# Optimization experiments

Hardware: AMD Instinct MI355X
Metric: run time of the kernel (lower is better)

The kernel has to match this reference:

```python
import math
import jax, jax.numpy as jnp
import numpy as np

B, LQ, LK, D, H = 4, 2048, 2048, 512, 8  # dim_Q=dim_K=dim_V=D, num_heads=H


def _layernorm(x, g, b, eps=1e-5):
    mu = jnp.mean(x, axis=-1, keepdims=True)
    var = jnp.var(x, axis=-1, keepdims=True)
    return (x - mu) * jax.lax.rsqrt(var + eps) * g + b


def setup_inputs() -> dict:
    key = jax.random.key(0)
    ks = jax.random.split(key, 16)
    s = 1.0 / math.sqrt(D)
    return {
        "Q": jax.random.normal(ks[0], (B, LQ, D), jnp.float32),
        "K": jax.random.normal(ks[1], (B, LK, D), jnp.float32),
        "pad_mask": jax.random.randint(ks[2], (B, LK), 0, 2, jnp.int32),
        "Wq": jax.random.normal(ks[3], (D, D), jnp.float32) * s,
        "bq": jnp.zeros((D,), jnp.float32),
        "Wk": jax.random.normal(ks[4], (D, D), jnp.float32) * s,
        "bk": jnp.zeros((D,), jnp.float32),
        "Wv": jax.random.normal(ks[5], (D, D), jnp.float32) * s,
        "bv": jnp.zeros((D,), jnp.float32),
        "Wo": jax.random.normal(ks[6], (D, D), jnp.float32) * s,
        "bo": jnp.zeros((D,), jnp.float32),
        "g0": jnp.ones((D,), jnp.float32),
        "b0": jnp.zeros((D,), jnp.float32),
        "g1": jnp.ones((D,), jnp.float32),
        "b1": jnp.zeros((D,), jnp.float32),
    }


def reference(Q, K, pad_mask, Wq, bq, Wk, bk, Wv, bv, Wo, bo, g0, b0, g1, b1):
    d = D // H  # head dim (torch: split(dim_split, 2) then cat along batch)
    Qh = (Q @ Wq + bq).reshape(B, LQ, H, d)
    Kh = (K @ Wk + bk).reshape(B, LK, H, d)
    Vh = (K @ Wv + bv).reshape(B, LK, H, d)
    # NOTE: original scales by sqrt(dim_V), not sqrt(head_dim)
    score = jnp.einsum('bqhd,bkhd->bhqk', Qh, Kh) / np.float32(math.sqrt(D))
    m = pad_mask[:, None, None, :].astype(score.dtype)  # (B,1,1,Lk)
    score = jnp.where(m == 0, jnp.float32(-1e12), score)
    A = jax.nn.softmax(score, axis=-1) * m  # post-softmax mask multiply (faithful)
    O = jnp.einsum('bhqk,bkhd->bqhd', A, Vh).reshape(B, LQ, D)
    O = Q + O
    O = _layernorm(O, g0, b0)
    O = O + jax.nn.relu(O @ Wo + bo)
    O = _layernorm(O, g1, b1)
    return O
```

## Files before the change

kernel.cpp:

```cpp
#include <hip/hip_runtime.h>
#include <math.h>

#define NB   4
#define SLQ  2048
#define SLK  2048
#define DIM  512
#define NH   8
#define HD   64
#define NROWS (NB * SLQ)
#define NT   (SLK / 64)

typedef __attribute__((ext_vector_type(8)))  __bf16 bf16x8;
typedef __attribute__((ext_vector_type(4)))  __bf16 bf16x4;
typedef __attribute__((ext_vector_type(2)))  __bf16 bf16x2;
typedef __attribute__((ext_vector_type(4)))  float  f32x4;
typedef __attribute__((ext_vector_type(16))) float  f32x16;
typedef __attribute__((ext_vector_type(4)))  unsigned int u32x4;

typedef const __attribute__((address_space(1))) void* as1_cptr;
typedef __attribute__((address_space(3))) void*       as3_ptr;
__device__ __forceinline__ void async_ld16(const void* g, void* s) {
    __builtin_amdgcn_global_load_lds((as1_cptr)g, (as3_ptr)s, 16, 0, 0);
}

__global__ __launch_bounds__(256)
void transpose_w_kernel(const float* __restrict__ Wq, const float* __restrict__ Wk,
                        const float* __restrict__ Wv, const float* __restrict__ Wo,
                        const int* __restrict__ maskp,
                        __bf16* __restrict__ Wt, float* __restrict__ msentg) {
    const int m = blockIdx.z;
    const int t = threadIdx.x;
    if (m == 4) {
        const int idx = (blockIdx.y * 16 + blockIdx.x) * 256 + t;
        if (idx < NB * SLK) msentg[idx] = maskp[idx] ? 0.f : -1e30f;
        return;
    }
    __shared__ float Ls[32][33];
    const float* W = (m == 0) ? Wq : (m == 1) ? Wk : (m == 2) ? Wv : Wo;
    const int k0 = blockIdx.y * 32, n0 = blockIdx.x * 32;
    const int r  = t >> 3, c = (t & 7) * 4;

    const float4 v = *reinterpret_cast<const float4*>(&W[(size_t)(k0 + r) * DIM + n0 + c]);
    Ls[r][c + 0] = v.x; Ls[r][c + 1] = v.y; Ls[r][c + 2] = v.z; Ls[r][c + 3] = v.w;
    __syncthreads();

    const int n = t >> 3, k = (t & 7) * 4;
    bf16x4 o;
    o[0] = (__bf16)Ls[k + 0][n];
    o[1] = (__bf16)Ls[k + 1][n];
    o[2] = (__bf16)Ls[k + 2][n];
    o[3] = (__bf16)Ls[k + 3][n];
    *reinterpret_cast<bf16x4*>(&Wt[(size_t)(512 * m + n0 + n) * DIM + k0 + k]) = o;
}

__global__ __launch_bounds__(256)
void proj_mfma_kernel(const float* __restrict__ Qp, const float* __restrict__ Kp,
                      const __bf16* __restrict__ Wt,
                      const float* __restrict__ bq, const float* __restrict__ bk,
                      const float* __restrict__ bv,
                      __bf16* __restrict__ Qh, __bf16* __restrict__ Kh,
                      __bf16* __restrict__ VhT) {
    __shared__ __bf16 As[128][72];
    __shared__ __bf16 Bs[64][72];

    const int bx = blockIdx.x;
    const int mode = (bx < 8) ? 0 : (bx < 16) ? 1 : 2;
    const int cb   = bx - ((mode == 0) ? 0 : (mode == 1) ? 8 : 16);
    const float*  A    = (mode == 0) ? Qp : Kp;
    const __bf16* Bt   = Wt + (size_t)((mode == 0) ? 0 : (mode == 1) ? 512 : 1024) * DIM;
    const float*  bias = ((mode == 0) ? bq : (mode == 1) ? bk : bv) + cb * 64;
    const int col0 = cb * 64;

    const int t  = threadIdx.x;
    const int w  = t >> 6, l = t & 63, lg = l >> 4, lc = l & 15;
    const int wr = w >> 1, wc = w & 1;
    const int row0 = blockIdx.y * 128;

    f32x4 acc[4][2];
    #pragma unroll
    for (int mi = 0; mi < 4; ++mi)
        #pragma unroll
        for (int nj = 0; nj < 2; ++nj) acc[mi][nj] = f32x4{0.f, 0.f, 0.f, 0.f};

    const int sr = t >> 3, sc = (t & 7) * 8;

    for (int k0 = 0; k0 < DIM; k0 += 64) {
        __syncthreads();
        #pragma unroll
        for (int i = 0; i < 4; ++i) {
            const int r = i * 32 + sr;
            const float4 a0 = *reinterpret_cast<const float4*>(
                &A[(size_t)(row0 + r) * DIM + k0 + sc]);
            const float4 a1 = *reinterpret_cast<const float4*>(
                &A[(size_t)(row0 + r) * DIM + k0 + sc + 4]);
            bf16x8 hv;
            hv[0] = (__bf16)a0.x; hv[1] = (__bf16)a0.y;
            hv[2] = (__bf16)a0.z; hv[3] = (__bf16)a0.w;
            hv[4] = (__bf16)a1.x; hv[5] = (__bf16)a1.y;
            hv[6] = (__bf16)a1.z; hv[7] = (__bf16)a1.w;
            *reinterpret_cast<bf16x8*>(&As[r][sc]) = hv;
        }
        #pragma unroll
        for (int i = 0; i < 2; ++i) {
            const int n = i * 32 + sr;
            *reinterpret_cast<bf16x8*>(&Bs[n][sc]) =
                *reinterpret_cast<const bf16x8*>(&Bt[(size_t)(col0 + n) * DIM + k0 + sc]);
        }
        __syncthreads();

        #pragma unroll
        for (int ks = 0; ks < 2; ++ks) {
            bf16x8 af[4], bfv[2];
            #pragma unroll
            for (int mi = 0; mi < 4; ++mi)
                af[mi] = *reinterpret_cast<const bf16x8*>(
                    &As[wr * 64 + mi * 16 + lc][ks * 32 + lg * 8]);
            #pragma unroll
            for (int nj = 0; nj < 2; ++nj)
                bfv[nj] = *reinterpret_cast<const bf16x8*>(
                    &Bs[wc * 32 + nj * 16 + lc][ks * 32 + lg * 8]);
            #pragma unroll
            for (int mi = 0; mi < 4; ++mi)
                #pragma unroll
                for (int nj = 0; nj < 2; ++nj)
                    acc[mi][nj] = __builtin_amdgcn_mfma_f32_16x16x32_bf16(
                        af[mi], bfv[nj], acc[mi][nj], 0, 0, 0);
        }
    }

    #pragma unroll
    for (int mi = 0; mi < 4; ++mi) {
        #pragma unroll
        for (int nj = 0; nj < 2; ++nj) {
            const int cl  = wc * 32 + nj * 16 + lc;
            const float bb = bias[cl];
            if (mode == 2) {
                const int dcol = col0 + cl;
                const int hh = dcol >> 6, dd = dcol & 63;
                const int row = row0 + wr * 64 + mi * 16 + lg * 4;
                const int bi  = row >> 11, key = row & 2047;
                bf16x4 pk;
                #pragma unroll
                for (int r = 0; r < 4; ++r) pk[r] = (__bf16)(acc[mi][nj][r] + bb);
                *reinterpret_cast<bf16x4*>(
                    &VhT[((size_t)(bi * NH + hh) * HD + dd) * SLK + key]) = pk;
            } else {
                __bf16* out = (mode == 0) ? Qh : Kh;
                #pragma unroll
                for (int r = 0; r < 4; ++r) {
                    const int row = row0 + wr * 64 + mi * 16 + lg * 4 + r;
                    out[(size_t)row * DIM + col0 + cl] = (__bf16)(acc[mi][nj][r] + bb);
                }
            }
        }
    }
}

__global__ __launch_bounds__(256)
void ffn_mfma_kernel(const float* __restrict__ A, const __bf16* __restrict__ Bt,
                     const float* __restrict__ bias, float* __restrict__ outv) {
    __shared__ __bf16 As[128][72];
    __shared__ __bf16 Bs[64][72];

    const int t  = threadIdx.x;
    const int w  = t >> 6, l = t & 63, lg = l >> 4, lc = l & 15;
    const int wr = w >> 1, wc = w & 1;
    const int row0 = blockIdx.y * 128, col0 = blockIdx.x * 64;

    f32x4 acc[4][2];
    #pragma unroll
    for (int mi = 0; mi < 4; ++mi)
        #pragma unroll
        for (int nj = 0; nj < 2; ++nj) acc[mi][nj] = f32x4{0.f, 0.f, 0.f, 0.f};

    const int sr = t >> 3, sc = (t & 7) * 8;

    for (int k0 = 0; k0 < DIM; k0 += 64) {
        __syncthreads();
        #pragma unroll
        for (int i = 0; i < 4; ++i) {
            const int r = i * 32 + sr;
            const float4 a0 = *reinterpret_cast<const float4*>(
                &A[(size_t)(row0 + r) * DIM + k0 + sc]);
            const float4 a1 = *reinterpret_cast<const float4*>(
                &A[(size_t)(row0 + r) * DIM + k0 + sc + 4]);
            bf16x8 hv;
            hv[0] = (__bf16)a0.x; hv[1] = (__bf16)a0.y;
            hv[2] = (__bf16)a0.z; hv[3] = (__bf16)a0.w;
            hv[4] = (__bf16)a1.x; hv[5] = (__bf16)a1.y;
            hv[6] = (__bf16)a1.z; hv[7] = (__bf16)a1.w;
            *reinterpret_cast<bf16x8*>(&As[r][sc]) = hv;
        }
        #pragma unroll
        for (int i = 0; i < 2; ++i) {
            const int n = i * 32 + sr;
            *reinterpret_cast<bf16x8*>(&Bs[n][sc]) =
                *reinterpret_cast<const bf16x8*>(&Bt[(size_t)(col0 + n) * DIM + k0 + sc]);
        }
        __syncthreads();

        #pragma unroll
        for (int ks = 0; ks < 2; ++ks) {
            bf16x8 af[4], bfv[2];
            #pragma unroll
            for (int mi = 0; mi < 4; ++mi)
                af[mi] = *reinterpret_cast<const bf16x8*>(
                    &As[wr * 64 + mi * 16 + lc][ks * 32 + lg * 8]);
            #pragma unroll
            for (int nj = 0; nj < 2; ++nj)
                bfv[nj] = *reinterpret_cast<const bf16x8*>(
                    &Bs[wc * 32 + nj * 16 + lc][ks * 32 + lg * 8]);
            #pragma unroll
            for (int mi = 0; mi < 4; ++mi)
                #pragma unroll
                for (int nj = 0; nj < 2; ++nj)
                    acc[mi][nj] = __builtin_amdgcn_mfma_f32_16x16x32_bf16(
                        af[mi], bfv[nj], acc[mi][nj], 0, 0, 0);
        }
    }

    #pragma unroll
    for (int mi = 0; mi < 4; ++mi) {
        #pragma unroll
        for (int nj = 0; nj < 2; ++nj) {
            const int cl  = wc * 32 + nj * 16 + lc;
            const int col = col0 + cl;
            #pragma unroll
            for (int r = 0; r < 4; ++r) {
                const int row = row0 + wr * 64 + mi * 16 + lg * 4 + r;
                const float vv = acc[mi][nj][r] + bias[col];
                outv[(size_t)row * DIM + col] =
                    A[(size_t)row * DIM + col] + fmaxf(vv, 0.f);
            }
        }
    }
}

__global__ __launch_bounds__(256)
void attn_mfma_kernel(const __bf16* __restrict__ Qh, const __bf16* __restrict__ Kh,
                      const __bf16* __restrict__ VhT, const float* __restrict__ msentg,
                      float* __restrict__ Oa) {
    const int pos  = blockIdx.x;
    const int orig = (pos & 7) * 64 + (pos >> 3);
    const int qb = orig & 15;
    const int h  = (orig >> 4) & 7;
    const int b  = orig >> 7;

    const int tid = threadIdx.x;
    const int w   = tid >> 6;
    const int l   = tid & 63;
    const int ql  = l & 31;
    const int hi  = l >> 5;
    const int x7  = ql & 7;

    __shared__ __bf16 Ks[3][64][64];
    __shared__ __bf16 Vt[3][64][64];
    __shared__ float  msent[SLK];
    __shared__ float  linv[4][32];

    {
        const float* mb = msentg + b * SLK;
        #pragma unroll
        for (int i = 0; i < 2; ++i) {
            const int idx = (i * 256 + tid) * 4;
            *reinterpret_cast<f32x4*>(&msent[idx]) =
                *reinterpret_cast<const f32x4*>(&mb[idx]);
        }
    }

    const int q0 = qb * 128 + w * 32;
    bf16x8 qf[4];
    {
        const __bf16* qrow = Qh + (size_t)(b * SLQ + q0 + ql) * DIM + h * HD + hi * 8;
        #pragma unroll
        for (int c = 0; c < 4; ++c)
            qf[c] = *reinterpret_cast<const bf16x8*>(qrow + c * 16);
    }

    const __bf16* kbase = Kh  + (size_t)b * SLK * DIM + h * HD;
    const __bf16* vbase = VhT + (size_t)(b * NH + h) * HD * SLK;

    const int srow = l >> 3;
    const int schk = (l & 7) ^ srow;

    auto STAGE = [&](int nb_, int k0_) {
        #pragma unroll
        for (int i = 0; i < 2; ++i) {
            const int rb = w * 16 + i * 8;
            async_ld16(kbase + (size_t)(k0_ + rb + srow) * DIM + schk * 8,
                       &Ks[nb_][rb][0]);
            async_ld16(vbase + (size_t)(rb + srow) * SLK + k0_ + schk * 8,
                       &Vt[nb_][rb][0]);
        }
    };

    f32x16 oacc[2];
    #pragma unroll
    for (int i = 0; i < 16; ++i) { oacc[0][i] = 0.f; oacc[1][i] = 0.f; }
    float l_part = 0.f;
    const float scale2 = 0.06377551f;

    STAGE(0, 0);
    STAGE(1, 64);

    int rd = 0;
    for (int t = 0; t < NT; ++t) {
        if (t == NT - 1) asm volatile("s_waitcnt vmcnt(0)" ::: "memory");
        else             asm volatile("s_waitcnt vmcnt(4)" ::: "memory");
        __syncthreads();

        if (t + 2 < NT) {
            const int st = (rd + 2 >= 3) ? rd - 1 : rd + 2;
            STAGE(st, (t + 2) * 64);
        }

        const int k0 = t * 64;
        const __bf16* KsC = &Ks[rd][0][0];
        const __bf16* VtC = &Vt[rd][0][0];

        f32x16 sacc[2];
        #pragma unroll
        for (int i = 0; i < 16; ++i) { sacc[0][i] = 0.f; sacc[1][i] = 0.f; }
        #pragma unroll
        for (int kb = 0; kb < 2; ++kb) {
            #pragma unroll
            for (int c = 0; c < 4; ++c) {
                const bf16x8 kf = *reinterpret_cast<const bf16x8*>(
                    &KsC[(kb * 32 + ql) * 64 + (((2 * c + hi) ^ x7) << 3)]);
                sacc[kb] = __builtin_amdgcn_mfma_f32_32x32x16_bf16(
                    kf, qf[c], sacc[kb], 0, 0, 0);
            }
        }

        unsigned int P2[2][8];
        #pragma unroll
        for (int kb = 0; kb < 2; ++kb) {
            #pragma unroll
            for (int m = 0; m < 4; ++m) {
                const f32x4 tm = *reinterpret_cast<const f32x4*>(
                    &msent[k0 + kb * 32 + 8 * m + 4 * hi]);
                float p[4];
                #pragma unroll
                for (int j = 0; j < 4; ++j) {
                    p[j] = __builtin_amdgcn_exp2f(
                        fmaf(sacc[kb][4 * m + j], scale2, tm[j]));
                    l_part += p[j];
                }
                bf16x2 w0, w1;
                w0[0] = (__bf16)p[0]; w0[1] = (__bf16)p[1];
                w1[0] = (__bf16)p[2]; w1[1] = (__bf16)p[3];
                P2[kb][2 * m]     = __builtin_bit_cast(unsigned int, w0);
                P2[kb][2 * m + 1] = __builtin_bit_cast(unsigned int, w1);
            }
        }

        #pragma unroll
        for (int kb = 0; kb < 2; ++kb) {
            #pragma unroll
            for (int cc = 0; cc < 2; ++cc) {
                asm volatile("v_permlane32_swap_b32 %0, %1"
                             : "+v"(P2[kb][4 * cc + 0]), "+v"(P2[kb][4 * cc + 2]));
                asm volatile("v_permlane32_swap_b32 %0, %1"
                             : "+v"(P2[kb][4 * cc + 1]), "+v"(P2[kb][4 * cc + 3]));
            }
        }
        bf16x8 pfrag[4];
        #pragma unroll
        for (int c = 0; c < 4; ++c) {
            const int kb = c >> 1, cc = c & 1;
            u32x4 fw;
            fw.x = P2[kb][4 * cc + 0]; fw.y = P2[kb][4 * cc + 1];
            fw.z = P2[kb][4 * cc + 2]; fw.w = P2[kb][4 * cc + 3];
            pfrag[c] = __builtin_bit_cast(bf16x8, fw);
        }

        #pragma unroll
        for (int db = 0; db < 2; ++db) {
            #pragma unroll
            for (int c = 0; c < 4; ++c) {
                const bf16x8 vf = *reinterpret_cast<const bf16x8*>(
                    &VtC[(db * 32 + ql) * 64 + (((2 * c + hi) ^ x7) << 3)]);
                oacc[db] = __builtin_amdgcn_mfma_f32_32x32x16_bf16(
                    pfrag[c], vf, oacc[db], 0, 0, 0);
            }
        }

        rd = (rd == 2) ? 0 : rd + 1;
    }

    const float lsum = l_part + __shfl_xor(l_part, 32, 64);
    if (hi == 0) linv[w][ql] = (lsum > 0.f) ? 1.f / lsum : 0.f;
    #pragma unroll
    for (int db = 0; db < 2; ++db) {
        #pragma unroll
        for (int m = 0; m < 4; ++m) {
            const f32x4 iv = *reinterpret_cast<const f32x4*>(&linv[w][8 * m + 4 * hi]);
            #pragma unroll
            for (int j = 0; j < 4; ++j) {
                const int qr = 8 * m + 4 * hi + j;
                Oa[(size_t)(b * SLQ + q0 + qr) * DIM + h * HD + db * 32 + ql] =
                    oacc[db][4 * m + j] * iv[j];
            }
        }
    }
}

__device__ __forceinline__ float wave_sum(float v) {
    #pragma unroll
    for (int off = 32; off > 0; off >>= 1) v += __shfl_xor(v, off, 64);
    return v;
}

__global__ __launch_bounds__(256)
void ln_kernel(const float* X, const float* Y,
               const float* g, const float* bta, float* out) {
    const int w    = threadIdx.x >> 6;
    const int lane = threadIdx.x & 63;
    const int row  = blockIdx.x * 4 + w;
    const size_t base = (size_t)row * DIM + lane * 8;

    float v[8];
    *reinterpret_cast<float4*>(&v[0]) = *reinterpret_cast<const float4*>(&X[base]);
    *reinterpret_cast<float4*>(&v[4]) = *reinterpret_cast<const float4*>(&X[base + 4]);
    if (Y != nullptr) {
        const float4 y0 = *reinterpret_cast<const float4*>(&Y[base]);
        const float4 y1 = *reinterpret_cast<const float4*>(&Y[base + 4]);
        v[0] += y0.x; v[1] += y0.y; v[2] += y0.z; v[3] += y0.w;
        v[4] += y1.x; v[5] += y1.y; v[6] += y1.z; v[7] += y1.w;
    }

    float s = 0.f, ss = 0.f;
    #pragma unroll
    for (int i = 0; i < 8; ++i) { s += v[i]; ss += v[i] * v[i]; }
    s  = wave_sum(s);
    ss = wave_sum(ss);
    const float mean = s * (1.f / DIM);
    const float var  = ss * (1.f / DIM) - mean * mean;
    const float rstd = rsqrtf(var + 1e-5f);

    const float4 g0 = *reinterpret_cast<const float4*>(&g[lane * 8]);
    const float4 g1 = *reinterpret_cast<const float4*>(&g[lane * 8 + 4]);
    const float4 b0 = *reinterpret_cast<const float4*>(&bta[lane * 8]);
    const float4 b1 = *reinterpret_cast<const float4*>(&bta[lane * 8 + 4]);
    float gg[8] = {g0.x, g0.y, g0.z, g0.w, g1.x, g1.y, g1.z, g1.w};
    float bb[8] = {b0.x, b0.y, b0.z, b0.w, b1.x, b1.y, b1.z, b1.w};

    float4 o0, o1;
    o0.x = (v[0] - mean) * rstd * gg[0] + bb[0];
    o0.y = (v[1] - mean) * rstd * gg[1] + bb[1];
    o0.z = (v[2] - mean) * rstd * gg[2] + bb[2];
    o0.w = (v[3] - mean) * rstd * gg[3] + bb[3];
    o1.x = (v[4] - mean) * rstd * gg[4] + bb[4];
    o1.y = (v[5] - mean) * rstd * gg[5] + bb[5];
    o1.z = (v[6] - mean) * rstd * gg[6] + bb[6];
    o1.w = (v[7] - mean) * rstd * gg[7] + bb[7];
    *reinterpret_cast<float4*>(&out[base])     = o0;
    *reinterpret_cast<float4*>(&out[base + 4]) = o1;
}

extern "C" void kernel_launch(void* const* d_in, const int* in_sizes, int n_in,
                              void* d_out, int out_size, void* d_ws, size_t ws_size,
                              hipStream_t stream) {
    const float* Q     = (const float*)d_in[0];
    const float* K     = (const float*)d_in[1];
    const int*   maskp = (const int*)  d_in[2];
    const float* Wq    = (const float*)d_in[3];
    const float* bq    = (const float*)d_in[4];
    const float* Wk    = (const float*)d_in[5];
    const float* bk    = (const float*)d_in[6];
    const float* Wv    = (const float*)d_in[7];
    const float* bv    = (const float*)d_in[8];
    const float* Wo    = (const float*)d_in[9];
    const float* bo    = (const float*)d_in[10];
    const float* g0    = (const float*)d_in[11];
    const float* b0    = (const float*)d_in[12];
    const float* g1    = (const float*)d_in[13];
    const float* b1    = (const float*)d_in[14];

    float* out = (float*)d_out;
    char*  ws  = (char*)d_ws;
    __bf16* Qh     = (__bf16*)ws;
    __bf16* Kh     = (__bf16*)(ws + (8u  << 20));
    __bf16* VhT    = (__bf16*)(ws + (16u << 20));
    __bf16* Wt     = (__bf16*)(ws + (24u << 20));
    float*  H1     = (float*)(ws + (26u << 20));
    float*  msentg = (float*)(ws + (42u << 20));
    float*  R2     = (float*)ws;
    float*  Oa     = out;

    transpose_w_kernel<<<dim3(16, 16, 5), 256, 0, stream>>>(
        Wq, Wk, Wv, Wo, maskp, Wt, msentg);

    proj_mfma_kernel<<<dim3(24, 64), 256, 0, stream>>>(
        Q, K, Wt, bq, bk, bv, Qh, Kh, VhT);

    attn_mfma_kernel<<<dim3(512), 256, 0, stream>>>(Qh, Kh, VhT, msentg, Oa);

    ln_kernel<<<NROWS / 4, 256, 0, stream>>>(Oa, Q, g0, b0, H1);

    ffn_mfma_kernel<<<dim3(8, 64), 256, 0, stream>>>(
        H1, Wt + (size_t)1536 * DIM, bo, R2);

    ln_kernel<<<NROWS / 4, 256, 0, stream>>>(R2, nullptr, g1, b1, out);
}
```

Before: 145.5 us.

## Split attention along the key dimension into two halves and combine in layernorm

The attention kernel now splits each (batch, head, query-block) task into two key halves, doubling the grid from 512 to 1024 blocks. Each half writes unnormalized partial outputs and row sums, and a new fused layernorm kernel adds the halves, normalizes, adds the residual and applies LN0. This works because the softmax uses a fixed offset with no running max, so the partial sums add directly. The aim is better occupancy across the GPU's compute units; the cost is extra global traffic for the second partial buffer and the sums. It also adds s_setprio around the MFMA sections and replaces __syncthreads with a raw barrier.

```diff
diff --git a/kernel.cpp b/kernel.cpp
--- a/kernel.cpp
+++ b/kernel.cpp
@@ -8,7 +8,7 @@
 #define NH   8
 #define HD   64
 #define NROWS (NB * SLQ)
-#define NT   (SLK / 64)
+#define NTH  16
 
 typedef __attribute__((ext_vector_type(8)))  __bf16 bf16x8;
 typedef __attribute__((ext_vector_type(4)))  __bf16 bf16x4;
@@ -239,12 +239,14 @@
 __global__ __launch_bounds__(256)
 void attn_mfma_kernel(const __bf16* __restrict__ Qh, const __bf16* __restrict__ Kh,
                       const __bf16* __restrict__ VhT, const float* __restrict__ msentg,
-                      float* __restrict__ Oa) {
+                      float* __restrict__ O0, float* __restrict__ O1,
+                      float* __restrict__ l0b, float* __restrict__ l1b) {
     const int pos  = blockIdx.x;
-    const int orig = (pos & 7) * 64 + (pos >> 3);
-    const int qb = orig & 15;
-    const int h  = (orig >> 4) & 7;
-    const int b  = orig >> 7;
+    const int orig = (pos & 7) * 128 + (pos >> 3);
+    const int half = orig & 1;
+    const int qb   = (orig >> 1) & 15;
+    const int h    = (orig >> 5) & 7;
+    const int b    = orig >> 8;
 
     const int tid = threadIdx.x;
     const int w   = tid >> 6;
@@ -255,17 +257,12 @@
 
     __shared__ __bf16 Ks[3][64][64];
     __shared__ __bf16 Vt[3][64][64];
-    __shared__ float  msent[SLK];
-    __shared__ float  linv[4][32];
+    __shared__ float  msent[1024];
 
     {
-        const float* mb = msentg + b * SLK;
-        #pragma unroll
-        for (int i = 0; i < 2; ++i) {
-            const int idx = (i * 256 + tid) * 4;
-            *reinterpret_cast<f32x4*>(&msent[idx]) =
-                *reinterpret_cast<const f32x4*>(&mb[idx]);
-        }
+        const float* mb = msentg + b * SLK + half * 1024;
+        *reinterpret_cast<f32x4*>(&msent[tid * 4]) =
+            *reinterpret_cast<const f32x4*>(&mb[tid * 4]);
     }
 
     const int q0 = qb * 128 + w * 32;
@@ -277,8 +274,8 @@
             qf[c] = *reinterpret_cast<const bf16x8*>(qrow + c * 16);
     }
 
-    const __bf16* kbase = Kh  + (size_t)b * SLK * DIM + h * HD;
-    const __bf16* vbase = VhT + (size_t)(b * NH + h) * HD * SLK;
+    const __bf16* kbase = Kh  + ((size_t)b * SLK + half * 1024) * DIM + h * HD;
+    const __bf16* vbase = VhT + (size_t)(b * NH + h) * HD * SLK + half * 1024;
 
     const int srow = l >> 3;
     const int schk = (l & 7) ^ srow;
@@ -302,14 +299,15 @@
 
     STAGE(0, 0);
     STAGE(1, 64);
+    asm volatile("s_waitcnt lgkmcnt(0)" ::: "memory");
 
     int rd = 0;
-    for (int t = 0; t < NT; ++t) {
-        if (t == NT - 1) asm volatile("s_waitcnt vmcnt(0)" ::: "memory");
-        else             asm volatile("s_waitcnt vmcnt(4)" ::: "memory");
-        __syncthreads();
-
-        if (t + 2 < NT) {
+    for (int t = 0; t < NTH; ++t) {
+        if (t == NTH - 1) asm volatile("s_waitcnt vmcnt(0)" ::: "memory");
+        else              asm volatile("s_waitcnt vmcnt(4)" ::: "memory");
+        __builtin_amdgcn_s_barrier();
+
+        if (t + 2 < NTH) {
             const int st = (rd + 2 >= 3) ? rd - 1 : rd + 2;
             STAGE(st, (t + 2) * 64);
         }
@@ -321,6 +319,7 @@
         f32x16 sacc[2];
         #pragma unroll
         for (int i = 0; i < 16; ++i) { sacc[0][i] = 0.f; sacc[1][i] = 0.f; }
+        __builtin_amdgcn_s_setprio(1);
         #pragma unroll
         for (int kb = 0; kb < 2; ++kb) {
             #pragma unroll
@@ -331,6 +330,7 @@
                     kf, qf[c], sacc[kb], 0, 0, 0);
             }
         }
+        __builtin_amdgcn_s_setprio(0);
 
         unsigned int P2[2][8];
         #pragma unroll
@@ -374,6 +374,7 @@
             pfrag[c] = __builtin_bit_cast(bf16x8, fw);
         }
 
+        __builtin_amdgcn_s_setprio(1);
         #pragma unroll
         for (int db = 0; db < 2; ++db) {
             #pragma unroll
@@ -384,22 +385,24 @@
                     pfrag[c], vf, oacc[db], 0, 0, 0);
             }
         }
+        __builtin_amdgcn_s_setprio(0);
 
         rd = (rd == 2) ? 0 : rd + 1;
     }
 
+    float* Op = half ? O1 : O0;
+    float* lb = half ? l1b : l0b;
     const float lsum = l_part + __shfl_xor(l_part, 32, 64);
-    if (hi == 0) linv[w][ql] = (lsum > 0.f) ? 1.f / lsum : 0.f;
+    if (hi == 0) lb[(size_t)(b * SLQ + q0 + ql) * NH + h] = lsum;
     #pragma unroll
     for (int db = 0; db < 2; ++db) {
         #pragma unroll
         for (int m = 0; m < 4; ++m) {
-            const f32x4 iv = *reinterpret_cast<const f32x4*>(&linv[w][8 * m + 4 * hi]);
             #pragma unroll
             for (int j = 0; j < 4; ++j) {
                 const int qr = 8 * m + 4 * hi + j;
-                Oa[(size_t)(b * SLQ + q0 + qr) * DIM + h * HD + db * 32 + ql] =
-                    oacc[db][4 * m + j] * iv[j];
+                Op[(size_t)(b * SLQ + q0 + qr) * DIM + h * HD + db * 32 + ql] =
+                    oacc[db][4 * m + j];
             }
         }
     }
@@ -412,8 +415,68 @@
 }
 
 __global__ __launch_bounds__(256)
-void ln_kernel(const float* X, const float* Y,
-               const float* g, const float* bta, float* out) {
+void ln_combine_kernel(const float* X0, const float* X1,
+                       const float* l0b, const float* l1b,
+                       const float* Y, const float* g, const float* bta,
+                       float* out) {
+    const int w    = threadIdx.x >> 6;
+    const int lane = threadIdx.x & 63;
+    const int row  = blockIdx.x * 4 + w;
+    const int head = lane >> 3;
+    const size_t base = (size_t)row * DIM + lane * 8;
+
+    const float ls = l0b[(size_t)row * NH + head] + l1b[(size_t)row * NH + head];
+    const float inv = (ls > 0.f) ? 1.f / ls : 0.f;
+
+    float v[8];
+    {
+        const float4 a0 = *reinterpret_cast<const float4*>(&X0[base]);
+        const float4 a1 = *reinterpret_cast<const float4*>(&X0[base + 4]);
+        const float4 c0 = *reinterpret_cast<const float4*>(&X1[base]);
+        const float4 c1 = *reinterpret_cast<const float4*>(&X1[base + 4]);
+        const float4 y0 = *reinterpret_cast<const float4*>(&Y[base]);
+        const float4 y1 = *reinterpret_cast<const float4*>(&Y[base + 4]);
+        v[0] = (a0.x + c0.x) * inv + y0.x;
+        v[1] = (a0.y + c0.y) * inv + y0.y;
+        v[2] = (a0.z + c0.z) * inv + y0.z;
+        v[3] = (a0.w + c0.w) * inv + y0.w;
+        v[4] = (a1.x + c1.x) * inv + y1.x;
+        v[5] = (a1.y + c1.y) * inv + y1.y;
+        v[6] = (a1.z + c1.z) * inv + y1.z;
+        v[7] = (a1.w + c1.w) * inv + y1.w;
+    }
+
+    float s = 0.f, ss = 0.f;
+    #pragma unroll
+    for (int i = 0; i < 8; ++i) { s += v[i]; ss += v[i] * v[i]; }
+    s  = wave_sum(s);
+    ss = wave_sum(ss);
+    const float mean = s * (1.f / DIM);
+    const float var  = ss * (1.f / DIM) - mean * mean;
+    const float rstd = rsqrtf(var + 1e-5f);
+
+    const float4 g0 = *reinterpret_cast<const float4*>(&g[lane * 8]);
+    const float4 g1 = *reinterpret_cast<const float4*>(&g[lane * 8 + 4]);
+    const float4 b0 = *reinterpret_cast<const float4*>(&bta[lane * 8]);
+    const float4 b1 = *reinterpret_cast<const float4*>(&bta[lane * 8 + 4]);
+    float gg[8] = {g0.x, g0.y, g0.z, g0.w, g1.x, g1.y, g1.z, g1.w};
+    float bb[8] = {b0.x, b0.y, b0.z, b0.w, b1.x, b1.y, b1.z, b1.w};
+
+    float4 o0, o1;
+    o0.x = (v[0] - mean) * rstd * gg[0] + bb[0];
+    o0.y = (v[1] - mean) * rstd * gg[1] + bb[1];
+    o0.z = (v[2] - mean) * rstd * gg[2] + bb[2];
+    o0.w = (v[3] - mean) * rstd * gg[3] + bb[3];
+    o1.x = (v[4] - mean) * rstd * gg[4] + bb[4];
+    o1.y = (v[5] - mean) * rstd * gg[5] + bb[5];
+    o1.z = (v[6] - mean) * rstd * gg[6] + bb[6];
+    o1.w = (v[7] - mean) * rstd * gg[7] + bb[7];
+    *reinterpret_cast<float4*>(&out[base])     = o0;
+    *reinterpret_cast<float4*>(&out[base + 4]) = o1;
+}
+
+__global__ __launch_bounds__(256)
+void ln_kernel(const float* X, const float* g, const float* bta, float* out) {
     const int w    = threadIdx.x >> 6;
     const int lane = threadIdx.x & 63;
     const int row  = blockIdx.x * 4 + w;
@@ -422,12 +485,6 @@
     float v[8];
     *reinterpret_cast<float4*>(&v[0]) = *reinterpret_cast<const float4*>(&X[base]);
     *reinterpret_cast<float4*>(&v[4]) = *reinterpret_cast<const float4*>(&X[base + 4]);
-    if (Y != nullptr) {
-        const float4 y0 = *reinterpret_cast<const float4*>(&Y[base]);
-        const float4 y1 = *reinterpret_cast<const float4*>(&Y[base + 4]);
-        v[0] += y0.x; v[1] += y0.y; v[2] += y0.z; v[3] += y0.w;
-        v[4] += y1.x; v[5] += y1.y; v[6] += y1.z; v[7] += y1.w;
-    }
 
     float s = 0.f, ss = 0.f;
     #pragma unroll
@@ -483,10 +540,13 @@
     __bf16* Kh     = (__bf16*)(ws + (8u  << 20));
     __bf16* VhT    = (__bf16*)(ws + (16u << 20));
     __bf16* Wt     = (__bf16*)(ws + (24u << 20));
-    float*  H1     = (float*)(ws + (26u << 20));
+    float*  O1     = (float*)(ws + (26u << 20));
     float*  msentg = (float*)(ws + (42u << 20));
-    float*  R2     = (float*)ws;
-    float*  Oa     = out;
+    float*  l0b    = (float*)(ws + (42u << 20) + (64u << 10));
+    float*  l1b    = (float*)(ws + (42u << 20) + (320u << 10));
+    float*  H1     = (float*)ws;
+    float*  R2     = (float*)(ws + (26u << 20));
+    float*  O0     = out;
 
     transpose_w_kernel<<<dim3(16, 16, 5), 256, 0, stream>>>(
         Wq, Wk, Wv, Wo, maskp, Wt, msentg);
@@ -494,12 +554,14 @@
     proj_mfma_kernel<<<dim3(24, 64), 256, 0, stream>>>(
         Q, K, Wt, bq, bk, bv, Qh, Kh, VhT);
 
-    attn_mfma_kernel<<<dim3(512), 256, 0, stream>>>(Qh, Kh, VhT, msentg, Oa);
-
-    ln_kernel<<<NROWS / 4, 256, 0, stream>>>(Oa, Q, g0, b0, H1);
+    attn_mfma_kernel<<<dim3(1024), 256, 0, stream>>>(
+        Qh, Kh, VhT, msentg, O0, O1, l0b, l1b);
+
+    ln_combine_kernel<<<NROWS / 4, 256, 0, stream>>>(
+        O0, O1, l0b, l1b, Q, g0, b0, H1);
 
     ffn_mfma_kernel<<<dim3(8, 64), 256, 0, stream>>>(
         H1, Wt + (size_t)1536 * DIM, bo, R2);
 
-    ln_kernel<<<NROWS / 4, 256, 0, stream>>>(R2, nullptr, g1, b1, out);
-}
+    ln_kernel<<<NROWS / 4, 256, 0, stream>>>(R2, g1, b1, out);
+}
```

Measured after the change: 150.0 us. +3.1%, slower.

## Store attention output and LN1 result in bf16; add MFMA priority hints

Applied to the files above, without the earlier changes.

The attention output and the first layernorm output are now written as bf16 rather than fp32, which halves the memory traffic between attention, LN1 and the FFN GEMM. The FFN kernel also no longer converts fp32 to bf16 while staging A. The attention loop swaps __syncthreads for a raw s_barrier after an explicit lgkmcnt wait, and wraps its MFMA blocks in s_setprio. The cost is extra rounding: the FFN residual now uses the bf16 LN1 value instead of fp32.

```diff
diff --git a/kernel.cpp b/kernel.cpp
--- a/kernel.cpp
+++ b/kernel.cpp
@@ -157,7 +157,7 @@
 }
 
 __global__ __launch_bounds__(256)
-void ffn_mfma_kernel(const float* __restrict__ A, const __bf16* __restrict__ Bt,
+void ffn_mfma_kernel(const __bf16* __restrict__ A, const __bf16* __restrict__ Bt,
                      const float* __restrict__ bias, float* __restrict__ outv) {
     __shared__ __bf16 As[128][72];
     __shared__ __bf16 Bs[64][72];
@@ -180,16 +180,8 @@
         #pragma unroll
         for (int i = 0; i < 4; ++i) {
             const int r = i * 32 + sr;
-            const float4 a0 = *reinterpret_cast<const float4*>(
-                &A[(size_t)(row0 + r) * DIM + k0 + sc]);
-            const float4 a1 = *reinterpret_cast<const float4*>(
-                &A[(size_t)(row0 + r) * DIM + k0 + sc + 4]);
-            bf16x8 hv;
-            hv[0] = (__bf16)a0.x; hv[1] = (__bf16)a0.y;
-            hv[2] = (__bf16)a0.z; hv[3] = (__bf16)a0.w;
-            hv[4] = (__bf16)a1.x; hv[5] = (__bf16)a1.y;
-            hv[6] = (__bf16)a1.z; hv[7] = (__bf16)a1.w;
-            *reinterpret_cast<bf16x8*>(&As[r][sc]) = hv;
+            *reinterpret_cast<bf16x8*>(&As[r][sc]) =
+                *reinterpret_cast<const bf16x8*>(&A[(size_t)(row0 + r) * DIM + k0 + sc]);
         }
         #pragma unroll
         for (int i = 0; i < 2; ++i) {
@@ -230,7 +222,7 @@
                 const int row = row0 + wr * 64 + mi * 16 + lg * 4 + r;
                 const float vv = acc[mi][nj][r] + bias[col];
                 outv[(size_t)row * DIM + col] =
-                    A[(size_t)row * DIM + col] + fmaxf(vv, 0.f);
+                    (float)A[(size_t)row * DIM + col] + fmaxf(vv, 0.f);
             }
         }
     }
@@ -239,7 +231,7 @@
 __global__ __launch_bounds__(256)
 void attn_mfma_kernel(const __bf16* __restrict__ Qh, const __bf16* __restrict__ Kh,
                       const __bf16* __restrict__ VhT, const float* __restrict__ msentg,
-                      float* __restrict__ Oa) {
+                      __bf16* __restrict__ Oa) {
     const int pos  = blockIdx.x;
     const int orig = (pos & 7) * 64 + (pos >> 3);
     const int qb = orig & 15;
@@ -302,12 +294,13 @@
 
     STAGE(0, 0);
     STAGE(1, 64);
+    asm volatile("s_waitcnt lgkmcnt(0)" ::: "memory");
 
     int rd = 0;
     for (int t = 0; t < NT; ++t) {
         if (t == NT - 1) asm volatile("s_waitcnt vmcnt(0)" ::: "memory");
         else             asm volatile("s_waitcnt vmcnt(4)" ::: "memory");
-        __syncthreads();
+        __builtin_amdgcn_s_barrier();
 
         if (t + 2 < NT) {
             const int st = (rd + 2 >= 3) ? rd - 1 : rd + 2;
@@ -321,6 +314,7 @@
         f32x16 sacc[2];
         #pragma unroll
         for (int i = 0; i < 16; ++i) { sacc[0][i] = 0.f; sacc[1][i] = 0.f; }
+        __builtin_amdgcn_s_setprio(1);
         #pragma unroll
         for (int kb = 0; kb < 2; ++kb) {
             #pragma unroll
@@ -331,6 +325,7 @@
                     kf, qf[c], sacc[kb], 0, 0, 0);
             }
         }
+        __builtin_amdgcn_s_setprio(0);
 
         unsigned int P2[2][8];
         #pragma unroll
@@ -374,6 +369,7 @@
             pfrag[c] = __builtin_bit_cast(bf16x8, fw);
         }
 
+        __builtin_amdgcn_s_setprio(1);
         #pragma unroll
         for (int db = 0; db < 2; ++db) {
             #pragma unroll
@@ -384,6 +380,7 @@
                     pfrag[c], vf, oacc[db], 0, 0, 0);
             }
         }
+        __builtin_amdgcn_s_setprio(0);
 
         rd = (rd == 2) ? 0 : rd + 1;
     }
@@ -399,7 +396,7 @@
             for (int j = 0; j < 4; ++j) {
                 const int qr = 8 * m + 4 * hi + j;
                 Oa[(size_t)(b * SLQ + q0 + qr) * DIM + h * HD + db * 32 + ql] =
-                    oacc[db][4 * m + j] * iv[j];
+                    (__bf16)(oacc[db][4 * m + j] * iv[j]);
             }
         }
     }
@@ -412,22 +409,55 @@
 }
 
 __global__ __launch_bounds__(256)
-void ln_kernel(const float* X, const float* Y,
-               const float* g, const float* bta, float* out) {
+void ln1_kernel(const __bf16* X, const float* Y,
+                const float* g, const float* bta, __bf16* out) {
     const int w    = threadIdx.x >> 6;
     const int lane = threadIdx.x & 63;
     const int row  = blockIdx.x * 4 + w;
     const size_t base = (size_t)row * DIM + lane * 8;
 
+    const bf16x8 xv = *reinterpret_cast<const bf16x8*>(&X[base]);
+    const float4 y0 = *reinterpret_cast<const float4*>(&Y[base]);
+    const float4 y1 = *reinterpret_cast<const float4*>(&Y[base + 4]);
+    float v[8];
+    v[0] = (float)xv[0] + y0.x; v[1] = (float)xv[1] + y0.y;
+    v[2] = (float)xv[2] + y0.z; v[3] = (float)xv[3] + y0.w;
+    v[4] = (float)xv[4] + y1.x; v[5] = (float)xv[5] + y1.y;
+    v[6] = (float)xv[6] + y1.z; v[7] = (float)xv[7] + y1.w;
+
+    float s = 0.f, ss = 0.f;
+    #pragma unroll
+    for (int i = 0; i < 8; ++i) { s += v[i]; ss += v[i] * v[i]; }
+    s  = wave_sum(s);
+    ss = wave_sum(ss);
+    const float mean = s * (1.f / DIM);
+    const float var  = ss * (1.f / DIM) - mean * mean;
+    const float rstd = rsqrtf(var + 1e-5f);
+
+    const float4 g0 = *reinterpret_cast<const float4*>(&g[lane * 8]);
+    const float4 g1 = *reinterpret_cast<const float4*>(&g[lane * 8 + 4]);
+    const float4 b0 = *reinterpret_cast<const float4*>(&bta[lane * 8]);
+    const float4 b1 = *reinterpret_cast<const float4*>(&bta[lane * 8 + 4]);
+    float gg[8] = {g0.x, g0.y, g0.z, g0.w, g1.x, g1.y, g1.z, g1.w};
+    float bb[8] = {b0.x, b0.y, b0.z, b0.w, b1.x, b1.y, b1.z, b1.w};
+
+    bf16x8 o;
+    #pragma unroll
+    for (int i = 0; i < 8; ++i)
+        o[i] = (__bf16)((v[i] - mean) * rstd * gg[i] + bb[i]);
+    *reinterpret_cast<bf16x8*>(&out[base]) = o;
+}
+
+__global__ __launch_bounds__(256)
+void ln2_kernel(const float* X, const float* g, const float* bta, float* out) {
+    const int w    = threadIdx.x >> 6;
+    const int lane = threadIdx.x & 63;
+    const int row  = blockIdx.x * 4 + w;
+    const size_t base = (size_t)row * DIM + lane * 8;
+
     float v[8];
     *reinterpret_cast<float4*>(&v[0]) = *reinterpret_cast<const float4*>(&X[base]);
     *reinterpret_cast<float4*>(&v[4]) = *reinterpret_cast<const float4*>(&X[base + 4]);
-    if (Y != nullptr) {
-        const float4 y0 = *reinterpret_cast<const float4*>(&Y[base]);
-        const float4 y1 = *reinterpret_cast<const float4*>(&Y[base + 4]);
-        v[0] += y0.x; v[1] += y0.y; v[2] += y0.z; v[3] += y0.w;
-        v[4] += y1.x; v[5] += y1.y; v[6] += y1.z; v[7] += y1.w;
-    }
 
     float s = 0.f, ss = 0.f;
     #pragma unroll
@@ -483,10 +513,10 @@
     __bf16* Kh     = (__bf16*)(ws + (8u  << 20));
     __bf16* VhT    = (__bf16*)(ws + (16u << 20));
     __bf16* Wt     = (__bf16*)(ws + (24u << 20));
-    float*  H1     = (float*)(ws + (26u << 20));
+    __bf16* Oa     = (__bf16*)(ws + (26u << 20));
+    __bf16* H1     = (__bf16*)(ws + (34u << 20));
     float*  msentg = (float*)(ws + (42u << 20));
     float*  R2     = (float*)ws;
-    float*  Oa     = out;
 
     transpose_w_kernel<<<dim3(16, 16, 5), 256, 0, stream>>>(
         Wq, Wk, Wv, Wo, maskp, Wt, msentg);
@@ -496,10 +526,10 @@
 
     attn_mfma_kernel<<<dim3(512), 256, 0, stream>>>(Qh, Kh, VhT, msentg, Oa);
 
-    ln_kernel<<<NROWS / 4, 256, 0, stream>>>(Oa, Q, g0, b0, H1);
+    ln1_kernel<<<NROWS / 4, 256, 0, stream>>>(Oa, Q, g0, b0, H1);
 
     ffn_mfma_kernel<<<dim3(8, 64), 256, 0, stream>>>(
         H1, Wt + (size_t)1536 * DIM, bo, R2);
 
-    ln_kernel<<<NROWS / 4, 256, 0, stream>>>(R2, nullptr, g1, b1, out);
-}
+    ln2_kernel<<<NROWS / 4, 256, 0, stream>>>(R2, g1, b1, out);
+}
```

Result: no change. 145.1 us (-0.2%).
